# Kernel tuning notes

Measured on AMD Instinct MI355X. Metric: run time of the kernel, lower is better.

The kernel has to match this reference:

```python
import jax, jax.numpy as jnp
import numpy as np

N_NODES = 50000
N_EDGES = 800000
NUM_RELS = 16
IN_DIM = 16      # == NUM_RELS (one-hot of op_class_id)
H_DIM = 128
OUT_DIM = 128    # must equal H_DIM (actor/critic consume output-layer root feats)
LIN_DIM = 512


def setup_inputs() -> dict:
    key = jax.random.key(0)
    ks = jax.random.split(key, 16)
    op_class_id = jax.random.randint(ks[0], (N_NODES,), 0, NUM_RELS, dtype=jnp.int32)
    norm = jax.random.uniform(ks[1], (N_NODES,), dtype=jnp.float32)
    src = jax.random.randint(ks[2], (N_EDGES,), 0, N_NODES, dtype=jnp.int32)
    dst = jax.random.randint(ks[3], (N_EDGES,), 0, N_NODES, dtype=jnp.int32)
    s = 0.1
    W0 = jax.random.normal(ks[4], (NUM_RELS, IN_DIM, H_DIM), jnp.float32) * s
    W1 = jax.random.normal(ks[5], (NUM_RELS, H_DIM, H_DIM), jnp.float32) * s
    W2 = jax.random.normal(ks[6], (NUM_RELS, H_DIM, OUT_DIM), jnp.float32) * s
    a1_w = jax.random.normal(ks[7], (OUT_DIM, LIN_DIM), jnp.float32) * s
    a1_b = jnp.zeros((LIN_DIM,), jnp.float32)
    a2_w = jax.random.normal(ks[8], (LIN_DIM, OUT_DIM), jnp.float32) * s
    a2_b = jnp.zeros((OUT_DIM,), jnp.float32)
    c1_w = jax.random.normal(ks[9], (OUT_DIM, LIN_DIM), jnp.float32) * s
    c1_b = jnp.zeros((LIN_DIM,), jnp.float32)
    c2_w = jax.random.normal(ks[10], (LIN_DIM, 1), jnp.float32) * s
    c2_b = jnp.zeros((1,), jnp.float32)
    return dict(op_class_id=op_class_id, norm=norm, src=src, dst=dst,
                W0=W0, W1=W1, W2=W2,
                a1_w=a1_w, a1_b=a1_b, a2_w=a2_w, a2_b=a2_b,
                c1_w=c1_w, c1_b=c1_b, c2_w=c2_w, c2_b=c2_b)


def _rgcn_layer(h, cls, norm, src, dst, W, act):
    # per-node relation-specific transform: h[n] @ W[cls[n]]
    # compute all relations then select (R small, avoids [N,in,out] gather)
    stacked = jnp.einsum('ni,rio->rno', h, W)          # [R, N, out]
    msg = stacked[cls, jnp.arange(h.shape[0])]         # [N, out]
    msg = msg * norm[:, None]
    agg = jax.ops.segment_sum(msg[src], dst, num_segments=h.shape[0])
    return act(agg)


def reference(op_class_id, norm, src, dst, W0, W1, W2,
              a1_w, a1_b, a2_w, a2_b, c1_w, c1_b, c2_w, c2_b):
    one_hot = jax.nn.one_hot(op_class_id, IN_DIM, dtype=jnp.float32)  # op_class_one_hot
    h = _rgcn_layer(one_hot, op_class_id, norm, src, dst, W0, jax.nn.relu)
    h = _rgcn_layer(h, op_class_id, norm, src, dst, W1, jax.nn.relu)
    h = _rgcn_layer(h, op_class_id, norm, src, dst, W2,
                    lambda x: jax.nn.softmax(x, axis=1))
    root = h[0]                                        # [OUT_DIM]
    probs = jax.nn.relu(root @ a1_w + a1_b) @ a2_w + a2_b
    value = jax.nn.relu(root @ c1_w + c1_b) @ c2_w + c2_b
    return probs, value
```

## Files before the change

kernel.cpp:

```cpp
#include <hip/hip_runtime.h>

#define NN 50000
#define NE 800000
#define NR 16
#define HD 128
#define LIND 512

#define CAP1 1024
#define CAP0 4096
#define E0CAP 4096
#define E1CAP 32768

#define C_N1 0
#define C_N0 1
#define C_E0 2
#define C_E1 3

#define PZ ((int)0xAAAAAAAA)

__global__ void k_scanA(const int* __restrict__ src, const int* __restrict__ dst,
                        int* map1, int* e0_src, int* cnt) {
    int tid = blockIdx.x * blockDim.x + threadIdx.x;
    int stride = gridDim.x * blockDim.x;
    const int4* d4p = (const int4*)dst;
    for (int q = tid; q < NE / 4; q += stride) {
        int4 d4 = d4p[q];
        int ds[4] = {d4.x, d4.y, d4.z, d4.w};
        #pragma unroll
        for (int j = 0; j < 4; j++) {
            if (ds[j] == 0) {
                int s = src[4 * q + j];
                int i = atomicAdd(&cnt[C_E0], 1) - PZ;
                if (i >= 0 && i < E0CAP) e0_src[i] = s;
                if (atomicCAS(&map1[s], PZ, -2) == PZ) {
                    int slot = atomicAdd(&cnt[C_N1], 1) - PZ;
                    map1[s] = (slot >= 0 && slot < CAP1) ? slot + 2 : 1;
                }
            }
        }
    }
}

__global__ void k_scanB1(const int* __restrict__ src, const int* __restrict__ dst,
                         const int* __restrict__ map1, int* map0,
                         int* e1_src, int* e1_dn, int* cnt) {
    int tid = blockIdx.x * blockDim.x + threadIdx.x;
    int stride = gridDim.x * blockDim.x;
    const int4* d4p = (const int4*)dst;
    for (int q = tid; q < NE / 4; q += stride) {
        int4 d4 = d4p[q];
        int ds[4] = {d4.x, d4.y, d4.z, d4.w};
        #pragma unroll
        for (int j = 0; j < 4; j++) {
            int m = map1[ds[j]];
            if (m >= 2) {
                int s = src[4 * q + j];
                int i = atomicAdd(&cnt[C_E1], 1) - PZ;
                if (i >= 0 && i < E1CAP) { e1_src[i] = s; e1_dn[i] = m - 2; }
                if (atomicCAS(&map0[s], PZ, -2) == PZ) {
                    int slot = atomicAdd(&cnt[C_N0], 1) - PZ;
                    map0[s] = (slot >= 0 && slot < CAP0) ? slot + 2 : 1;
                }
            }
        }
    }
}

__global__ void k_scanB2(const int* __restrict__ src, const int* __restrict__ dst,
                         const int* __restrict__ map0, const int* __restrict__ cls,
                         const float* __restrict__ norm, float* w0sum) {
    int tid = blockIdx.x * blockDim.x + threadIdx.x;
    int stride = gridDim.x * blockDim.x;
    const int4* d4p = (const int4*)dst;
    for (int q = tid; q < NE / 4; q += stride) {
        int4 d4 = d4p[q];
        int ds[4] = {d4.x, d4.y, d4.z, d4.w};
        #pragma unroll
        for (int j = 0; j < 4; j++) {
            int m = map0[ds[j]];
            if (m >= 2) {
                int s = src[4 * q + j];
                atomicAdd(&w0sum[((size_t)(m - 2) << 4) + cls[s]], norm[s]);
            }
        }
    }
}

__global__ void __launch_bounds__(128)
k_edge1(const int* __restrict__ cnt, const int* __restrict__ e1_src,
        const int* __restrict__ e1_dn, const int* __restrict__ map0,
        const int* __restrict__ cls, const float* __restrict__ norm,
        const float* __restrict__ W0, const float* __restrict__ W1,
        const float* __restrict__ w0sum, float* agg1) {
    int t = threadIdx.x;
    int e1n = cnt[C_E1] - PZ;
    if (e1n < 0) e1n = 0; if (e1n > E1CAP) e1n = E1CAP;
    __shared__ float shw[NR];
    __shared__ float sha[HD];
    for (int ei = blockIdx.x; ei < e1n; ei += gridDim.x) {
        int s = e1_src[ei];
        int dn = e1_dn[ei];
        int c = cls[s];
        float nm = norm[s];
        int sslot = map0[s] - 2;
        if (sslot < 0 || sslot >= CAP0) continue;
        if (t < NR) shw[t] = w0sum[((size_t)sslot << 4) + t];
        __syncthreads();
        float a = 0.f;
        #pragma unroll
        for (int cc = 0; cc < NR; cc++) a = fmaf(shw[cc], W0[cc * 2176 + t], a);
        sha[t] = fmaxf(a, 0.f);
        __syncthreads();
        const float* w = W1 + c * (HD * HD) + t;
        float acc = 0.f;
        #pragma unroll 16
        for (int i = 0; i < HD; i++) acc = fmaf(sha[i], w[i << 7], acc);
        atomicAdd(&agg1[((size_t)dn << 7) + t], acc * nm);
        __syncthreads();
    }
}

__global__ void __launch_bounds__(256)
k_tail2(const int* __restrict__ cnt, const int* __restrict__ e0_src,
        const int* __restrict__ map1, const int* __restrict__ cls,
        const float* __restrict__ norm, const float* __restrict__ agg1,
        const float* __restrict__ W2, float* rootpre, int* done,
        const float* __restrict__ a1w, const float* __restrict__ a1b,
        const float* __restrict__ a2w, const float* __restrict__ a2b,
        const float* __restrict__ c1w, const float* __restrict__ c1b,
        const float* __restrict__ c2w, const float* __restrict__ c2b,
        float* out) {
    const int t = threadIdx.x;
    const int b = blockIdx.x;

    if (b < NR) {
        const int c = b;
        __shared__ float u[HD];
        __shared__ int   sl[256];
        __shared__ int   sc[256];
        __shared__ float sn[256];
        __shared__ int any;
        if (t < HD) u[t] = 0.f;
        if (t == 0) any = 0;
        __syncthreads();
        int e0n = cnt[C_E0] - PZ;
        if (e0n < 0) e0n = 0; if (e0n > E0CAP) e0n = E0CAP;
        for (int base = 0; base < e0n; base += 256) {
            int nchunk = e0n - base; if (nchunk > 256) nchunk = 256;
            if (t < nchunk) {
                int s = e0_src[base + t];
                sl[t] = map1[s] - 2;
                sc[t] = cls[s];
                sn[t] = norm[s];
            }
            __syncthreads();
            for (int i = 0; i < nchunk; i++) {
                if (sc[i] != c) continue;
                int slot = sl[i];
                if (slot < 0 || slot >= CAP1) continue;
                if (t < HD) u[t] += sn[i] * fmaxf(agg1[((size_t)slot << 7) + t], 0.f);
                if (t == 0) any = 1;
            }
            __syncthreads();
        }
        if (any) {
            int o = t & 127, hf = t >> 7, k0 = hf << 6;
            const float* w2 = W2 + c * (HD * HD);
            float acc = 0.f;
            #pragma unroll 16
            for (int k = k0; k < k0 + 64; k++) acc = fmaf(u[k], w2[(k << 7) + o], acc);
            atomicAdd(&rootpre[o], acc);
        }
        __syncthreads();
        if (t == 0)
            __hip_atomic_fetch_add(&done[0], 1, __ATOMIC_RELEASE, __HIP_MEMORY_SCOPE_AGENT);
    } else {
        const int bb = b - NR;
        const int m = bb >> 3, g = bb & 7, k0 = g << 6;
        const float* Wh = m ? c1w : a1w;
        const float* bh = m ? c1b : a1b;
        const int o1 = t & 63, qu = t >> 6, kk1 = qu << 5;
        float wreg[32];
        #pragma unroll
        for (int i = 0; i < 32; i++) wreg[i] = Wh[(kk1 + i) * LIND + k0 + o1];
        float breg = bh[k0 + o1];
        const int o2 = t & 127, hf2 = t >> 7, j2 = hf2 << 5;
        float vreg[32];
        if (m == 0) {
            #pragma unroll
            for (int j = 0; j < 32; j++) vreg[j] = a2w[(k0 + j2 + j) * HD + o2];
        } else {
            vreg[0] = c2w[k0 + o1];
        }
        __shared__ float sha[HD];
        __shared__ float shz[64];
        __shared__ float red[256];
        if (t == 0) {
            while (__hip_atomic_load(&done[0], __ATOMIC_ACQUIRE,
                                     __HIP_MEMORY_SCOPE_AGENT) - PZ < NR)
                __builtin_amdgcn_s_sleep(2);
        }
        __syncthreads();
        if (t < HD)
            sha[t] = __hip_atomic_load(&rootpre[t], __ATOMIC_RELAXED,
                                       __HIP_MEMORY_SCOPE_AGENT);
        __syncthreads();
        float mx = -3.0e38f;
        for (int i = 0; i < HD; i++) mx = fmaxf(mx, sha[i]);
        float ex = (t < HD) ? expf(sha[t] - mx) : 0.f;
        __syncthreads();
        if (t < HD) sha[t] = ex;
        __syncthreads();
        float sum = 0.f;
        for (int i = 0; i < HD; i++) sum += sha[i];
        __syncthreads();
        if (t < HD) sha[t] = ex / sum;
        __syncthreads();
        {
            float z = 0.f;
            #pragma unroll
            for (int i = 0; i < 32; i++) z = fmaf(sha[kk1 + i], wreg[i], z);
            red[t] = z;
            __syncthreads();
            if (t < 64)
                shz[t] = fmaxf(breg * 0.f + bh[k0 + t] + red[t] + red[t + 64] + red[t + 128] + red[t + 192], 0.f);
        }
        __syncthreads();
        if (m == 0) {
            float acc = 0.f;
            #pragma unroll
            for (int j = 0; j < 32; j++) acc = fmaf(shz[j2 + j], vreg[j], acc);
            red[t] = acc;
            __syncthreads();
            if (t < HD) {
                float v = red[t] + red[t + 128];
                if (bb == 0) v += a2b[t];
                atomicAdd(&out[t], v);
            }
        } else {
            if (t < 64) red[t] = shz[t] * vreg[0];
            __syncthreads();
            if (t == 0) {
                float v = (bb == 8) ? c2b[0] : 0.f;
                for (int j = 0; j < 64; j++) v += red[j];
                atomicAdd(&out[HD], v);
            }
        }
    }
}

extern "C" void kernel_launch(void* const* d_in, const int* in_sizes, int n_in,
                              void* d_out, int out_size, void* d_ws, size_t ws_size,
                              hipStream_t stream) {
    const int*   cls  = (const int*)d_in[0];
    const float* norm = (const float*)d_in[1];
    const int*   src  = (const int*)d_in[2];
    const int*   dst  = (const int*)d_in[3];
    const float* W0   = (const float*)d_in[4];
    const float* W1   = (const float*)d_in[5];
    const float* W2   = (const float*)d_in[6];
    const float* a1w  = (const float*)d_in[7];
    const float* a1b  = (const float*)d_in[8];
    const float* a2w  = (const float*)d_in[9];
    const float* a2b  = (const float*)d_in[10];
    const float* c1w  = (const float*)d_in[11];
    const float* c1b  = (const float*)d_in[12];
    const float* c2w  = (const float*)d_in[13];
    const float* c2b  = (const float*)d_in[14];
    float* out = (float*)d_out;

    char* ws = (char*)d_ws;
    int*   cnt     = (int*)(ws + 0);
    int*   map1    = (int*)(ws + 64);
    int*   map0    = (int*)(ws + 200064);
    int*   e0_src  = (int*)(ws + 400064);
    int*   e1_src  = (int*)(ws + 416448);
    int*   e1_dn   = (int*)(ws + 547520);
    float* rootpre = (float*)(ws + 678592);
    float* w0sum   = (float*)(ws + 679104);
    float* agg1    = (float*)(ws + 941248);
    int*   done    = (int*)(ws + 1500032);

    k_scanA<<<1024, 256, 0, stream>>>(src, dst, map1, e0_src, cnt);
    k_scanB1<<<1024, 256, 0, stream>>>(src, dst, map1, map0, e1_src, e1_dn, cnt);
    k_scanB2<<<1024, 256, 0, stream>>>(src, dst, map0, cls, norm, w0sum);
    k_edge1<<<256, 128, 0, stream>>>(cnt, e1_src, e1_dn, map0, cls, norm, W0, W1, w0sum, agg1);
    k_tail2<<<NR + 16, 256, 0, stream>>>(cnt, e0_src, map1, cls, norm, agg1, W2,
                                         rootpre, done,
                                         a1w, a1b, a2w, a2b, c1w, c1b, c2w, c2b, out);
}
```

Baseline: 131.7 us.

## Fuse five-kernel pipeline into one cooperative kernel with grid syncs

Replaces the five separate launches (three edge scans, edge-1 transform, tail MLP) with a single cooperative kernel of 256 blocks that uses grid.sync between phases. The aim is to remove per-launch overhead and inter-kernel gaps. In exchange, the scans run on a smaller grid than the 1024 blocks used before, and each grid barrier has its own cost. The old multi-kernel path is kept as a fallback if the cooperative launch fails, and one line of the fallback critic reduction is changed.

```diff
diff --git a/kernel.cpp b/kernel.cpp
--- a/kernel.cpp
+++ b/kernel.cpp
@@ -1,4 +1,7 @@
 #include <hip/hip_runtime.h>
+#include <hip/hip_cooperative_groups.h>
+
+namespace cg = cooperative_groups;
 
 #define NN 50000
 #define NE 800000
@@ -17,6 +20,237 @@
 #define C_E1 3
 
 #define PZ ((int)0xAAAAAAAA)
+
+#define GRID_BLKS 256
+
+struct KParams {
+    const int*   cls;  const float* norm;
+    const int*   src;  const int*   dst;
+    const float* W0;   const float* W1;   const float* W2;
+    const float* a1w;  const float* a1b;  const float* a2w;  const float* a2b;
+    const float* c1w;  const float* c1b;  const float* c2w;  const float* c2b;
+    int*   cnt;  int* map1; int* map0;
+    int*   e0_src; int* e1_src; int* e1_dn;
+    float* rootpre; float* w0sum; float* agg1;
+    int*   done; float* out;
+};
+
+__global__ void __launch_bounds__(256, 2)
+k_fused(KParams p) {
+    const int t = threadIdx.x;
+    const int b = blockIdx.x;
+    const int tid = b * 256 + t;
+    const int stride = GRID_BLKS * 256;
+    cg::grid_group grid = cg::this_grid();
+
+    __shared__ union {
+        struct { float shw[NR]; float sha[HD]; } e1;
+        struct { float u[HD]; int sl[256]; int sc[256]; float sn[256]; int any; } rt;
+        struct { float sha[HD]; float shz[64]; float red[256]; } mlp;
+    } sm;
+
+    {
+        const int4* d4p = (const int4*)p.dst;
+        for (int q = tid; q < NE / 4; q += stride) {
+            int4 d4 = d4p[q];
+            int ds[4] = {d4.x, d4.y, d4.z, d4.w};
+            #pragma unroll
+            for (int j = 0; j < 4; j++) {
+                if (ds[j] == 0) {
+                    int s = p.src[4 * q + j];
+                    int i = atomicAdd(&p.cnt[C_E0], 1) - PZ;
+                    if (i >= 0 && i < E0CAP) p.e0_src[i] = s;
+                    if (atomicCAS(&p.map1[s], PZ, -2) == PZ) {
+                        int slot = atomicAdd(&p.cnt[C_N1], 1) - PZ;
+                        p.map1[s] = (slot >= 0 && slot < CAP1) ? slot + 2 : 1;
+                    }
+                }
+            }
+        }
+    }
+    grid.sync();
+
+    {
+        const int4* d4p = (const int4*)p.dst;
+        for (int q = tid; q < NE / 4; q += stride) {
+            int4 d4 = d4p[q];
+            int ds[4] = {d4.x, d4.y, d4.z, d4.w};
+            #pragma unroll
+            for (int j = 0; j < 4; j++) {
+                int m = p.map1[ds[j]];
+                if (m >= 2) {
+                    int s = p.src[4 * q + j];
+                    int i = atomicAdd(&p.cnt[C_E1], 1) - PZ;
+                    if (i >= 0 && i < E1CAP) { p.e1_src[i] = s; p.e1_dn[i] = m - 2; }
+                    if (atomicCAS(&p.map0[s], PZ, -2) == PZ) {
+                        int slot = atomicAdd(&p.cnt[C_N0], 1) - PZ;
+                        p.map0[s] = (slot >= 0 && slot < CAP0) ? slot + 2 : 1;
+                    }
+                }
+            }
+        }
+    }
+    grid.sync();
+
+    {
+        const int4* d4p = (const int4*)p.dst;
+        for (int q = tid; q < NE / 4; q += stride) {
+            int4 d4 = d4p[q];
+            int ds[4] = {d4.x, d4.y, d4.z, d4.w};
+            #pragma unroll
+            for (int j = 0; j < 4; j++) {
+                int mm = p.map0[ds[j]];
+                if (mm >= 2) {
+                    int s = p.src[4 * q + j];
+                    atomicAdd(&p.w0sum[((size_t)(mm - 2) << 4) + p.cls[s]], p.norm[s]);
+                }
+            }
+        }
+    }
+    grid.sync();
+
+    {
+        int e1n = p.cnt[C_E1] - PZ;
+        if (e1n < 0) e1n = 0; if (e1n > E1CAP) e1n = E1CAP;
+        for (int ei = b; ei < e1n; ei += GRID_BLKS) {
+            int s = p.e1_src[ei];
+            int dn = p.e1_dn[ei];
+            int c = p.cls[s];
+            float nm = p.norm[s];
+            int sslot = p.map0[s] - 2;
+            if (sslot < 0 || sslot >= CAP0) continue;
+            if (t < NR) sm.e1.shw[t] = p.w0sum[((size_t)sslot << 4) + t];
+            __syncthreads();
+            if (t < HD) {
+                float a = 0.f;
+                #pragma unroll
+                for (int cc = 0; cc < NR; cc++)
+                    a = fmaf(sm.e1.shw[cc], p.W0[cc * 2176 + t], a);
+                sm.e1.sha[t] = fmaxf(a, 0.f);
+            }
+            __syncthreads();
+            if (t < HD) {
+                const float* w = p.W1 + c * (HD * HD) + t;
+                float acc = 0.f;
+                #pragma unroll 16
+                for (int i = 0; i < HD; i++) acc = fmaf(sm.e1.sha[i], w[i << 7], acc);
+                atomicAdd(&p.agg1[((size_t)dn << 7) + t], acc * nm);
+            }
+            __syncthreads();
+        }
+    }
+    grid.sync();
+
+    if (b >= NR + 16) return;
+    if (b < NR) {
+        const int c = b;
+        if (t < HD) sm.rt.u[t] = 0.f;
+        if (t == 0) sm.rt.any = 0;
+        __syncthreads();
+        int e0n = p.cnt[C_E0] - PZ;
+        if (e0n < 0) e0n = 0; if (e0n > E0CAP) e0n = E0CAP;
+        for (int base = 0; base < e0n; base += 256) {
+            int nchunk = e0n - base; if (nchunk > 256) nchunk = 256;
+            if (t < nchunk) {
+                int s = p.e0_src[base + t];
+                sm.rt.sl[t] = p.map1[s] - 2;
+                sm.rt.sc[t] = p.cls[s];
+                sm.rt.sn[t] = p.norm[s];
+            }
+            __syncthreads();
+            for (int i = 0; i < nchunk; i++) {
+                if (sm.rt.sc[i] != c) continue;
+                int slot = sm.rt.sl[i];
+                if (slot < 0 || slot >= CAP1) continue;
+                if (t < HD) sm.rt.u[t] += sm.rt.sn[i] *
+                                fmaxf(p.agg1[((size_t)slot << 7) + t], 0.f);
+                if (t == 0) sm.rt.any = 1;
+            }
+            __syncthreads();
+        }
+        if (sm.rt.any) {
+            int o = t & 127, hf = t >> 7, k0 = hf << 6;
+            const float* w2 = p.W2 + c * (HD * HD);
+            float acc = 0.f;
+            #pragma unroll 16
+            for (int k = k0; k < k0 + 64; k++) acc = fmaf(sm.rt.u[k], w2[(k << 7) + o], acc);
+            atomicAdd(&p.rootpre[o], acc);
+        }
+        __syncthreads();
+        if (t == 0)
+            __hip_atomic_fetch_add(&p.done[0], 1, __ATOMIC_RELEASE, __HIP_MEMORY_SCOPE_AGENT);
+    } else {
+        const int bb = b - NR;
+        const int m = bb >> 3, g = bb & 7, k0 = g << 6;
+        const float* Wh = m ? p.c1w : p.a1w;
+        const float* bh = m ? p.c1b : p.a1b;
+        const int o1 = t & 63, qu = t >> 6, kk1 = qu << 5;
+        float wreg[32];
+        #pragma unroll
+        for (int i = 0; i < 32; i++) wreg[i] = Wh[(kk1 + i) * LIND + k0 + o1];
+        float breg = bh[k0 + o1];
+        const int o2 = t & 127, hf2 = t >> 7, j2 = hf2 << 5;
+        float vreg[32];
+        if (m == 0) {
+            #pragma unroll
+            for (int j = 0; j < 32; j++) vreg[j] = p.a2w[(k0 + j2 + j) * HD + o2];
+        } else {
+            vreg[0] = p.c2w[k0 + o1];
+        }
+        if (t == 0) {
+            while (__hip_atomic_load(&p.done[0], __ATOMIC_ACQUIRE,
+                                     __HIP_MEMORY_SCOPE_AGENT) - PZ < NR)
+                __builtin_amdgcn_s_sleep(2);
+        }
+        __syncthreads();
+        if (t < HD)
+            sm.mlp.sha[t] = __hip_atomic_load(&p.rootpre[t], __ATOMIC_RELAXED,
+                                              __HIP_MEMORY_SCOPE_AGENT);
+        __syncthreads();
+        float mx = -3.0e38f;
+        for (int i = 0; i < HD; i++) mx = fmaxf(mx, sm.mlp.sha[i]);
+        float ex = (t < HD) ? expf(sm.mlp.sha[t] - mx) : 0.f;
+        __syncthreads();
+        if (t < HD) sm.mlp.sha[t] = ex;
+        __syncthreads();
+        float sum = 0.f;
+        for (int i = 0; i < HD; i++) sum += sm.mlp.sha[i];
+        __syncthreads();
+        if (t < HD) sm.mlp.sha[t] = ex / sum;
+        __syncthreads();
+        {
+            float z = 0.f;
+            #pragma unroll
+            for (int i = 0; i < 32; i++) z = fmaf(sm.mlp.sha[kk1 + i], wreg[i], z);
+            sm.mlp.red[t] = z;
+            __syncthreads();
+            if (t < 64)
+                sm.mlp.shz[t] = fmaxf(breg + sm.mlp.red[t] + sm.mlp.red[t + 64]
+                                      + sm.mlp.red[t + 128] + sm.mlp.red[t + 192], 0.f);
+        }
+        __syncthreads();
+        if (m == 0) {
+            float acc = 0.f;
+            #pragma unroll
+            for (int j = 0; j < 32; j++) acc = fmaf(sm.mlp.shz[j2 + j], vreg[j], acc);
+            sm.mlp.red[t] = acc;
+            __syncthreads();
+            if (t < HD) {
+                float v = sm.mlp.red[t] + sm.mlp.red[t + 128];
+                if (bb == 0) v += p.a2b[t];
+                atomicAdd(&p.out[t], v);
+            }
+        } else {
+            if (t < 64) sm.mlp.red[t] = sm.mlp.shz[t] * vreg[0];
+            __syncthreads();
+            if (t == 0) {
+                float v = (bb == 8) ? p.c2b[0] : 0.f;
+                for (int j = 0; j < 64; j++) v += sm.mlp.red[j];
+                atomicAdd(&p.out[HD], v);
+            }
+        }
+    }
+}
 
 __global__ void k_scanA(const int* __restrict__ src, const int* __restrict__ dst,
                         int* map1, int* e0_src, int* cnt) {
@@ -242,7 +476,7 @@
             __syncthreads();
             if (t == 0) {
                 float v = (bb == 8) ? c2b[0] : 0.f;
-                for (int j = 0; j < 64; j++) v += red[j];
+                for (int j = 0; j < 64; j++) v += shz[j] * c2w[k0 + j];
                 atomicAdd(&out[HD], v);
             }
         }
@@ -281,11 +515,29 @@
     float* agg1    = (float*)(ws + 941248);
     int*   done    = (int*)(ws + 1500032);
 
-    k_scanA<<<1024, 256, 0, stream>>>(src, dst, map1, e0_src, cnt);
-    k_scanB1<<<1024, 256, 0, stream>>>(src, dst, map1, map0, e1_src, e1_dn, cnt);
-    k_scanB2<<<1024, 256, 0, stream>>>(src, dst, map0, cls, norm, w0sum);
-    k_edge1<<<256, 128, 0, stream>>>(cnt, e1_src, e1_dn, map0, cls, norm, W0, W1, w0sum, agg1);
-    k_tail2<<<NR + 16, 256, 0, stream>>>(cnt, e0_src, map1, cls, norm, agg1, W2,
-                                         rootpre, done,
-                                         a1w, a1b, a2w, a2b, c1w, c1b, c2w, c2b, out);
-}
+    KParams p;
+    p.cls = cls; p.norm = norm; p.src = src; p.dst = dst;
+    p.W0 = W0; p.W1 = W1; p.W2 = W2;
+    p.a1w = a1w; p.a1b = a1b; p.a2w = a2w; p.a2b = a2b;
+    p.c1w = c1w; p.c1b = c1b; p.c2w = c2w; p.c2b = c2b;
+    p.cnt = cnt; p.map1 = map1; p.map0 = map0;
+    p.e0_src = e0_src; p.e1_src = e1_src; p.e1_dn = e1_dn;
+    p.rootpre = rootpre; p.w0sum = w0sum; p.agg1 = agg1;
+    p.done = done; p.out = out;
+
+    void* args[] = { (void*)&p };
+    hipError_t err = hipLaunchCooperativeKernel(
+        reinterpret_cast<const void*>(k_fused),
+        dim3(GRID_BLKS), dim3(256), args, 0, stream);
+
+    if (err != hipSuccess) {
+        (void)hipGetLastError();
+        k_scanA<<<1024, 256, 0, stream>>>(src, dst, map1, e0_src, cnt);
+        k_scanB1<<<1024, 256, 0, stream>>>(src, dst, map1, map0, e1_src, e1_dn, cnt);
+        k_scanB2<<<1024, 256, 0, stream>>>(src, dst, map0, cls, norm, w0sum);
+        k_edge1<<<256, 128, 0, stream>>>(cnt, e1_src, e1_dn, map0, cls, norm, W0, W1, w0sum, agg1);
+        k_tail2<<<NR + 16, 256, 0, stream>>>(cnt, e0_src, map1, cls, norm, agg1, W2,
+                                             rootpre, done,
+                                             a1w, a1b, a2w, a2b, c1w, c1b, c2w, c2b, out);
+    }
+}
```

Result: slower. 268.0 us (+103.5%).

## Fuse scanB2, edge1 and tail kernels into one persistent kernel with grid barriers

Applied to the files above, without the earlier changes.

Merges the third edge scan, the layer-1 edge transform and the root/MLP tail into a single 512-block kernel, separated by software grid barriers built on atomic counters. This removes two kernel launch boundaries and their drain and refill gaps. In exchange, the code relies on all 512 blocks being co-resident to avoid deadlock. Shared memory is unioned across the phases, and the edge1 stage now runs on 256-thread blocks with half the threads idle.

```diff
diff --git a/kernel.cpp b/kernel.cpp
--- a/kernel.cpp
+++ b/kernel.cpp
@@ -15,8 +15,12 @@
 #define C_N0 1
 #define C_E0 2
 #define C_E1 3
+#define C_B1 4
+#define C_B2 5
 
 #define PZ ((int)0xAAAAAAAA)
+
+#define NB3 512
 
 __global__ void k_scanA(const int* __restrict__ src, const int* __restrict__ dst,
                         int* map1, int* e0_src, int* cnt) {
@@ -66,64 +70,14 @@
     }
 }
 
-__global__ void k_scanB2(const int* __restrict__ src, const int* __restrict__ dst,
-                         const int* __restrict__ map0, const int* __restrict__ cls,
-                         const float* __restrict__ norm, float* w0sum) {
-    int tid = blockIdx.x * blockDim.x + threadIdx.x;
-    int stride = gridDim.x * blockDim.x;
-    const int4* d4p = (const int4*)dst;
-    for (int q = tid; q < NE / 4; q += stride) {
-        int4 d4 = d4p[q];
-        int ds[4] = {d4.x, d4.y, d4.z, d4.w};
-        #pragma unroll
-        for (int j = 0; j < 4; j++) {
-            int m = map0[ds[j]];
-            if (m >= 2) {
-                int s = src[4 * q + j];
-                atomicAdd(&w0sum[((size_t)(m - 2) << 4) + cls[s]], norm[s]);
-            }
-        }
-    }
-}
-
-__global__ void __launch_bounds__(128)
-k_edge1(const int* __restrict__ cnt, const int* __restrict__ e1_src,
-        const int* __restrict__ e1_dn, const int* __restrict__ map0,
+__global__ void __launch_bounds__(256, 2)
+k_fuse3(const int* __restrict__ src, const int* __restrict__ dst,
         const int* __restrict__ cls, const float* __restrict__ norm,
+        const int* __restrict__ map0, const int* __restrict__ map1,
+        int* cnt, const int* __restrict__ e0_src,
+        const int* __restrict__ e1_src, const int* __restrict__ e1_dn,
+        float* w0sum, float* agg1,
         const float* __restrict__ W0, const float* __restrict__ W1,
-        const float* __restrict__ w0sum, float* agg1) {
-    int t = threadIdx.x;
-    int e1n = cnt[C_E1] - PZ;
-    if (e1n < 0) e1n = 0; if (e1n > E1CAP) e1n = E1CAP;
-    __shared__ float shw[NR];
-    __shared__ float sha[HD];
-    for (int ei = blockIdx.x; ei < e1n; ei += gridDim.x) {
-        int s = e1_src[ei];
-        int dn = e1_dn[ei];
-        int c = cls[s];
-        float nm = norm[s];
-        int sslot = map0[s] - 2;
-        if (sslot < 0 || sslot >= CAP0) continue;
-        if (t < NR) shw[t] = w0sum[((size_t)sslot << 4) + t];
-        __syncthreads();
-        float a = 0.f;
-        #pragma unroll
-        for (int cc = 0; cc < NR; cc++) a = fmaf(shw[cc], W0[cc * 2176 + t], a);
-        sha[t] = fmaxf(a, 0.f);
-        __syncthreads();
-        const float* w = W1 + c * (HD * HD) + t;
-        float acc = 0.f;
-        #pragma unroll 16
-        for (int i = 0; i < HD; i++) acc = fmaf(sha[i], w[i << 7], acc);
-        atomicAdd(&agg1[((size_t)dn << 7) + t], acc * nm);
-        __syncthreads();
-    }
-}
-
-__global__ void __launch_bounds__(256)
-k_tail2(const int* __restrict__ cnt, const int* __restrict__ e0_src,
-        const int* __restrict__ map1, const int* __restrict__ cls,
-        const float* __restrict__ norm, const float* __restrict__ agg1,
         const float* __restrict__ W2, float* rootpre, int* done,
         const float* __restrict__ a1w, const float* __restrict__ a1b,
         const float* __restrict__ a2w, const float* __restrict__ a2b,
@@ -132,16 +86,89 @@
         float* out) {
     const int t = threadIdx.x;
     const int b = blockIdx.x;
+    const int tid = b * 256 + t;
+    const int stride = NB3 * 256;
+
+    __shared__ union {
+        struct { float shw[NR]; float sha[HD]; } e1;
+        struct { float u[HD]; int sl[256]; int sc[256]; float sn[256]; int any; } rt;
+        struct { float sha[HD]; float shz[64]; float red[256]; } mlp;
+    } sm;
+
+    {
+        const int4* d4p = (const int4*)dst;
+        for (int q = tid; q < NE / 4; q += stride) {
+            int4 d4 = d4p[q];
+            int ds[4] = {d4.x, d4.y, d4.z, d4.w};
+            #pragma unroll
+            for (int j = 0; j < 4; j++) {
+                int mm = map0[ds[j]];
+                if (mm >= 2) {
+                    int s = src[4 * q + j];
+                    atomicAdd(&w0sum[((size_t)(mm - 2) << 4) + cls[s]], norm[s]);
+                }
+            }
+        }
+    }
+    __syncthreads();
+    if (t == 0) {
+        __hip_atomic_fetch_add(&cnt[C_B1], 1, __ATOMIC_RELEASE, __HIP_MEMORY_SCOPE_AGENT);
+        while (__hip_atomic_load(&cnt[C_B1], __ATOMIC_RELAXED,
+                                 __HIP_MEMORY_SCOPE_AGENT) - PZ < NB3)
+            __builtin_amdgcn_s_sleep(1);
+        (void)__hip_atomic_load(&cnt[C_B1], __ATOMIC_ACQUIRE, __HIP_MEMORY_SCOPE_AGENT);
+    }
+    __syncthreads();
+
+    {
+        int e1n = cnt[C_E1] - PZ;
+        if (e1n < 0) e1n = 0; if (e1n > E1CAP) e1n = E1CAP;
+        for (int ei = b; ei < e1n; ei += NB3) {
+            int s = e1_src[ei];
+            int dn = e1_dn[ei];
+            int c = cls[s];
+            float nm = norm[s];
+            int sslot = map0[s] - 2;
+            if (sslot < 0 || sslot >= CAP0) continue;
+            if (t < NR)
+                sm.e1.shw[t] = __hip_atomic_load(&w0sum[((size_t)sslot << 4) + t],
+                                                 __ATOMIC_RELAXED, __HIP_MEMORY_SCOPE_AGENT);
+            __syncthreads();
+            if (t < HD) {
+                float a = 0.f;
+                #pragma unroll
+                for (int cc = 0; cc < NR; cc++)
+                    a = fmaf(sm.e1.shw[cc], W0[cc * 2176 + t], a);
+                sm.e1.sha[t] = fmaxf(a, 0.f);
+            }
+            __syncthreads();
+            if (t < HD) {
+                const float* w = W1 + c * (HD * HD) + t;
+                float acc = 0.f;
+                #pragma unroll 16
+                for (int i = 0; i < HD; i++) acc = fmaf(sm.e1.sha[i], w[i << 7], acc);
+                atomicAdd(&agg1[((size_t)dn << 7) + t], acc * nm);
+            }
+            __syncthreads();
+        }
+    }
+    __syncthreads();
+    if (t == 0) {
+        __hip_atomic_fetch_add(&cnt[C_B2], 1, __ATOMIC_RELEASE, __HIP_MEMORY_SCOPE_AGENT);
+        if (b < NR) {
+            while (__hip_atomic_load(&cnt[C_B2], __ATOMIC_RELAXED,
+                                     __HIP_MEMORY_SCOPE_AGENT) - PZ < NB3)
+                __builtin_amdgcn_s_sleep(1);
+            (void)__hip_atomic_load(&cnt[C_B2], __ATOMIC_ACQUIRE, __HIP_MEMORY_SCOPE_AGENT);
+        }
+    }
+    __syncthreads();
+    if (b >= NR + 16) return;
 
     if (b < NR) {
         const int c = b;
-        __shared__ float u[HD];
-        __shared__ int   sl[256];
-        __shared__ int   sc[256];
-        __shared__ float sn[256];
-        __shared__ int any;
-        if (t < HD) u[t] = 0.f;
-        if (t == 0) any = 0;
+        if (t < HD) sm.rt.u[t] = 0.f;
+        if (t == 0) sm.rt.any = 0;
         __syncthreads();
         int e0n = cnt[C_E0] - PZ;
         if (e0n < 0) e0n = 0; if (e0n > E0CAP) e0n = E0CAP;
@@ -149,26 +176,30 @@
             int nchunk = e0n - base; if (nchunk > 256) nchunk = 256;
             if (t < nchunk) {
                 int s = e0_src[base + t];
-                sl[t] = map1[s] - 2;
-                sc[t] = cls[s];
-                sn[t] = norm[s];
+                sm.rt.sl[t] = map1[s] - 2;
+                sm.rt.sc[t] = cls[s];
+                sm.rt.sn[t] = norm[s];
             }
             __syncthreads();
             for (int i = 0; i < nchunk; i++) {
-                if (sc[i] != c) continue;
-                int slot = sl[i];
+                if (sm.rt.sc[i] != c) continue;
+                int slot = sm.rt.sl[i];
                 if (slot < 0 || slot >= CAP1) continue;
-                if (t < HD) u[t] += sn[i] * fmaxf(agg1[((size_t)slot << 7) + t], 0.f);
-                if (t == 0) any = 1;
-            }
-            __syncthreads();
-        }
-        if (any) {
+                if (t < HD) {
+                    float av = __hip_atomic_load(&agg1[((size_t)slot << 7) + t],
+                                                 __ATOMIC_RELAXED, __HIP_MEMORY_SCOPE_AGENT);
+                    sm.rt.u[t] += sm.rt.sn[i] * fmaxf(av, 0.f);
+                }
+                if (t == 0) sm.rt.any = 1;
+            }
+            __syncthreads();
+        }
+        if (sm.rt.any) {
             int o = t & 127, hf = t >> 7, k0 = hf << 6;
             const float* w2 = W2 + c * (HD * HD);
             float acc = 0.f;
             #pragma unroll 16
-            for (int k = k0; k < k0 + 64; k++) acc = fmaf(u[k], w2[(k << 7) + o], acc);
+            for (int k = k0; k < k0 + 64; k++) acc = fmaf(sm.rt.u[k], w2[(k << 7) + o], acc);
             atomicAdd(&rootpre[o], acc);
         }
         __syncthreads();
@@ -192,9 +223,6 @@
         } else {
             vreg[0] = c2w[k0 + o1];
         }
-        __shared__ float sha[HD];
-        __shared__ float shz[64];
-        __shared__ float red[256];
         if (t == 0) {
             while (__hip_atomic_load(&done[0], __ATOMIC_ACQUIRE,
                                      __HIP_MEMORY_SCOPE_AGENT) - PZ < NR)
@@ -202,47 +230,48 @@
         }
         __syncthreads();
         if (t < HD)
-            sha[t] = __hip_atomic_load(&rootpre[t], __ATOMIC_RELAXED,
-                                       __HIP_MEMORY_SCOPE_AGENT);
+            sm.mlp.sha[t] = __hip_atomic_load(&rootpre[t], __ATOMIC_RELAXED,
+                                              __HIP_MEMORY_SCOPE_AGENT);
         __syncthreads();
         float mx = -3.0e38f;
-        for (int i = 0; i < HD; i++) mx = fmaxf(mx, sha[i]);
-        float ex = (t < HD) ? expf(sha[t] - mx) : 0.f;
-        __syncthreads();
-        if (t < HD) sha[t] = ex;
+        for (int i = 0; i < HD; i++) mx = fmaxf(mx, sm.mlp.sha[i]);
+        float ex = (t < HD) ? expf(sm.mlp.sha[t] - mx) : 0.f;
+        __syncthreads();
+        if (t < HD) sm.mlp.sha[t] = ex;
         __syncthreads();
         float sum = 0.f;
-        for (int i = 0; i < HD; i++) sum += sha[i];
-        __syncthreads();
-        if (t < HD) sha[t] = ex / sum;
+        for (int i = 0; i < HD; i++) sum += sm.mlp.sha[i];
+        __syncthreads();
+        if (t < HD) sm.mlp.sha[t] = ex / sum;
         __syncthreads();
         {
             float z = 0.f;
             #pragma unroll
-            for (int i = 0; i < 32; i++) z = fmaf(sha[kk1 + i], wreg[i], z);
-            red[t] = z;
+            for (int i = 0; i < 32; i++) z = fmaf(sm.mlp.sha[kk1 + i], wreg[i], z);
+            sm.mlp.red[t] = z;
             __syncthreads();
             if (t < 64)
-                shz[t] = fmaxf(breg * 0.f + bh[k0 + t] + red[t] + red[t + 64] + red[t + 128] + red[t + 192], 0.f);
+                sm.mlp.shz[t] = fmaxf(breg + sm.mlp.red[t] + sm.mlp.red[t + 64]
+                                      + sm.mlp.red[t + 128] + sm.mlp.red[t + 192], 0.f);
         }
         __syncthreads();
         if (m == 0) {
             float acc = 0.f;
             #pragma unroll
-            for (int j = 0; j < 32; j++) acc = fmaf(shz[j2 + j], vreg[j], acc);
-            red[t] = acc;
+            for (int j = 0; j < 32; j++) acc = fmaf(sm.mlp.shz[j2 + j], vreg[j], acc);
+            sm.mlp.red[t] = acc;
             __syncthreads();
             if (t < HD) {
-                float v = red[t] + red[t + 128];
+                float v = sm.mlp.red[t] + sm.mlp.red[t + 128];
                 if (bb == 0) v += a2b[t];
                 atomicAdd(&out[t], v);
             }
         } else {
-            if (t < 64) red[t] = shz[t] * vreg[0];
+            if (t < 64) sm.mlp.red[t] = sm.mlp.shz[t] * vreg[0];
             __syncthreads();
             if (t == 0) {
                 float v = (bb == 8) ? c2b[0] : 0.f;
-                for (int j = 0; j < 64; j++) v += red[j];
+                for (int j = 0; j < 64; j++) v += sm.mlp.red[j];
                 atomicAdd(&out[HD], v);
             }
         }
@@ -283,9 +312,8 @@
 
     k_scanA<<<1024, 256, 0, stream>>>(src, dst, map1, e0_src, cnt);
     k_scanB1<<<1024, 256, 0, stream>>>(src, dst, map1, map0, e1_src, e1_dn, cnt);
-    k_scanB2<<<1024, 256, 0, stream>>>(src, dst, map0, cls, norm, w0sum);
-    k_edge1<<<256, 128, 0, stream>>>(cnt, e1_src, e1_dn, map0, cls, norm, W0, W1, w0sum, agg1);
-    k_tail2<<<NR + 16, 256, 0, stream>>>(cnt, e0_src, map1, cls, norm, agg1, W2,
-                                         rootpre, done,
-                                         a1w, a1b, a2w, a2b, c1w, c1b, c2w, c2b, out);
+    k_fuse3<<<NB3, 256, 0, stream>>>(src, dst, cls, norm, map0, map1, cnt,
+                                     e0_src, e1_src, e1_dn, w0sum, agg1,
+                                     W0, W1, W2, rootpre, done,
+                                     a1w, a1b, a2w, a2b, c1w, c1b, c2w, c2b, out);
 }
```

Measured after the change: 196.7 us. 49.4% more time.
